# Optimization experiments

Hardware: AMD Instinct MI355X
Metric: run time of the kernel (lower is better)

Reference implementation:

```python
import jax, jax.numpy as jnp
import numpy as np

TOPK = 30  # from init_kwargs


def setup_inputs() -> dict:
    key = jax.random.key(0)
    k1, k2, k3 = jax.random.split(key, 3)
    BH, N, D = 32, 2048, 64  # (batch*heads, seq_len, head_dim)
    return {
        "q": jax.random.normal(k1, (BH, N, D), dtype=jnp.float32),
        "k": jax.random.normal(k2, (BH, N, D), dtype=jnp.float32),
        "v": jax.random.normal(k3, (BH, N, D), dtype=jnp.float32),
        "B": 2048,          # == seq_len N (used for mask shape in original)
        "num_heads": 8,     # unused by the math, kept for signature parity
    }


def reference(q, k, v, B, num_heads):
    # scores: [BH, N, N]  (torch.bmm(q, k.transpose(1,2)))
    scores = jnp.einsum('bnd,bmd->bnm', q, k)
    # scale=None and attn_mask=None in the default call -> both branches skipped
    BH, N, _ = scores.shape
    # top-k per row, scatter 1.0 into a zero mask (faithful to torch.scatter_)
    _, idx = jax.lax.top_k(scores, TOPK)                      # [BH, N, TOPK]
    bi = jnp.arange(BH)[:, None, None]
    ri = jnp.arange(N)[None, :, None]
    keep = jnp.zeros((BH, N, N), dtype=bool).at[bi, ri, idx].set(True)
    # masked softmax over last axis (dim=2)
    masked = jnp.where(keep, scores, -jnp.inf)
    attn = jax.nn.softmax(masked, axis=-1)
    # dropout p=0.0 -> identity
    context = jnp.einsum('bnm,bmd->bnd', attn, v)
    return context, attn
```

## Files before the change

kernel.cpp:

```cpp
#include <hip/hip_runtime.h>
#include <hip/hip_bf16.h>

#define BHn 32
#define Nn 2048
#define Dn 64
#define KSEL 30
#define CAP 92
#define RB 64
#define CT 64
#define ZTH 1.90f

typedef short bf16x8 __attribute__((ext_vector_type(8)));
typedef float f32x4 __attribute__((ext_vector_type(4)));
typedef unsigned long long u64;

__device__ __forceinline__ unsigned ford(float x) {
  unsigned b = __float_as_uint(x);
  return (b & 0x80000000u) ? ~b : (b | 0x80000000u);
}
__device__ __forceinline__ float unford(unsigned u) {
  unsigned b = (u & 0x80000000u) ? (u & 0x7fffffffu) : ~u;
  return __uint_as_float(b);
}
__device__ __forceinline__ u64 umax64(u64 a, u64 b) { return a > b ? a : b; }

__device__ __forceinline__ void split2(float a, float b, ushort2& hi, ushort2& lo) {
  __hip_bfloat162 h = __float22bfloat162_rn(make_float2(a, b));
  union { __hip_bfloat162 v; ushort2 u; } ch; ch.v = h;
  hi = ch.u;
  float2 hf = __bfloat1622float2(h);
  __hip_bfloat162 l = __float22bfloat162_rn(make_float2(a - hf.x, b - hf.y));
  union { __hip_bfloat162 v; ushort2 u; } cl; cl.v = l;
  lo = cl.u;
}

__device__ __forceinline__ void pack8(float4 x0, float4 x1, bf16x8& hi, bf16x8& lo) {
  ushort2 h0, l0, h1, l1, h2, l2, h3, l3;
  split2(x0.x, x0.y, h0, l0); split2(x0.z, x0.w, h1, l1);
  split2(x1.x, x1.y, h2, l2); split2(x1.z, x1.w, h3, l3);
  hi = (bf16x8){(short)h0.x, (short)h0.y, (short)h1.x, (short)h1.y,
                (short)h2.x, (short)h2.y, (short)h3.x, (short)h3.y};
  lo = (bf16x8){(short)l0.x, (short)l0.y, (short)l1.x, (short)l1.y,
                (short)l2.x, (short)l2.y, (short)l3.x, (short)l3.y};
}

__global__ __launch_bounds__(256, 2) void score_select(
    const float* __restrict__ q, const float* __restrict__ k,
    const float* __restrict__ v, float* __restrict__ ctx,
    float* __restrict__ attn, unsigned* __restrict__ flags) {
  __shared__ ushort kh[CT][64], kl[CT][64];
  __shared__ u64 candL[RB][CAP];
  __shared__ unsigned ccnt[RB];
  __shared__ float tf[RB];

  const int t = threadIdx.x;
  const int bid = blockIdx.x;
  const int bh = (bid & 7) * 4 + ((bid >> 3) & 3);
  const int rb = bid >> 5;
  const int lane = t & 63, w = t >> 6;
  const int m16 = lane & 15, quad = lane >> 4;
  const int wr = w >> 1, wc = w & 1;

  const float* qb = q + ((size_t)bh * Nn + rb * RB) * Dn;
  const float* kb = k + (size_t)bh * Nn * Dn;
  const size_t growbase = (size_t)bh * Nn + (size_t)rb * RB;

  bf16x8 qaH[2][2], qaL[2][2];
#pragma unroll
  for (int ks = 0; ks < 2; ++ks)
#pragma unroll
    for (int mt = 0; mt < 2; ++mt) {
      const float* p = qb + (wr * 32 + mt * 16 + m16) * Dn + (ks * 4 + quad) * 8;
      float4 x0 = *(const float4*)p;
      float4 x1 = *(const float4*)(p + 4);
      pack8(x0, x1, qaH[ks][mt], qaL[ks][mt]);
    }

  if (t < RB) {
    const float* qr = qb + t * Dn;
    float ss = 0.f;
#pragma unroll
    for (int i = 0; i < 16; ++i) {
      float4 a = *(const float4*)(qr + i * 4);
      ss = fmaf(a.x, a.x, ss); ss = fmaf(a.y, a.y, ss);
      ss = fmaf(a.z, a.z, ss); ss = fmaf(a.w, a.w, ss);
    }
    tf[t] = ZTH * sqrtf(ss);
    ccnt[t] = 0u;
  }

  float4 pre[4];
#pragma unroll
  for (int i = 0; i < 4; ++i) {
    int c = t + 256 * i;
    pre[i] = *(const float4*)(kb + (size_t)(c >> 4) * Dn + (c & 15) * 4);
  }
  __syncthreads();

  unsigned tfr[2][4];
#pragma unroll
  for (int mt = 0; mt < 2; ++mt)
#pragma unroll
    for (int rg = 0; rg < 4; ++rg)
      tfr[mt][rg] = ford(tf[wr * 32 + mt * 16 + quad * 4 + rg]);

  for (int ct = 0; ct < Nn / CT; ++ct) {
#pragma unroll
    for (int i = 0; i < 4; ++i) {
      int c = t + 256 * i;
      int row = c >> 4, f4 = c & 15;
      float4 a = pre[i];
      int sp = (((f4 >> 1) ^ (row & 7)) << 1) | (f4 & 1);
      ushort2 h0, l0, h1, l1;
      split2(a.x, a.y, h0, l0);
      split2(a.z, a.w, h1, l1);
      *(ushort4*)&kh[row][sp * 4] = make_ushort4(h0.x, h0.y, h1.x, h1.y);
      *(ushort4*)&kl[row][sp * 4] = make_ushort4(l0.x, l0.y, l1.x, l1.y);
    }
    __syncthreads();

    if (ct + 1 < Nn / CT) {
#pragma unroll
      for (int i = 0; i < 4; ++i) {
        int c = t + 256 * i;
        pre[i] = *(const float4*)(kb + (size_t)((ct + 1) * CT + (c >> 4)) * Dn + (c & 15) * 4);
      }
    }

    f32x4 acc[2][2];
#pragma unroll
    for (int mt = 0; mt < 2; ++mt)
#pragma unroll
      for (int nt = 0; nt < 2; ++nt) acc[mt][nt] = (f32x4){0.f, 0.f, 0.f, 0.f};

#pragma unroll
    for (int ks = 0; ks < 2; ++ks) {
      bf16x8 bH[2], bL[2];
#pragma unroll
      for (int nt = 0; nt < 2; ++nt) {
        int rr = wc * 32 + nt * 16 + m16;
        int ch = (ks * 4 + quad) ^ (rr & 7);
        bH[nt] = *(const bf16x8*)&kh[rr][ch * 8];
        bL[nt] = *(const bf16x8*)&kl[rr][ch * 8];
      }
#pragma unroll
      for (int mt = 0; mt < 2; ++mt)
#pragma unroll
        for (int nt = 0; nt < 2; ++nt) {
          acc[mt][nt] = __builtin_amdgcn_mfma_f32_16x16x32_bf16(qaL[ks][mt], bH[nt], acc[mt][nt], 0, 0, 0);
          acc[mt][nt] = __builtin_amdgcn_mfma_f32_16x16x32_bf16(qaH[ks][mt], bL[nt], acc[mt][nt], 0, 0, 0);
          acc[mt][nt] = __builtin_amdgcn_mfma_f32_16x16x32_bf16(qaH[ks][mt], bH[nt], acc[mt][nt], 0, 0, 0);
        }
    }

#pragma unroll
    for (int mt = 0; mt < 2; ++mt)
#pragma unroll
      for (int rg = 0; rg < 4; ++rg) {
        unsigned tk = tfr[mt][rg];
        int rl = wr * 32 + mt * 16 + quad * 4 + rg;
#pragma unroll
        for (int nt = 0; nt < 2; ++nt) {
          float s = acc[mt][nt][rg];
          unsigned fk = ford(s);
          if (fk > tk) {
            unsigned pos = atomicAdd(&ccnt[rl], 1u);
            if (pos < CAP) {
              int col = ct * CT + wc * 32 + nt * 16 + m16;
              candL[rl][pos] = ((u64)fk << 32) | (unsigned)(2047 - col);
            }
          }
        }
      }
    __syncthreads();
  }

  const float* vb = v + (size_t)bh * Nn * Dn;
  for (int i = 0; i < RB / 4; ++i) {
    const int rl = w * 16 + i;
    const size_t gr = growbase + rl;
    const int C = (int)ccnt[rl];
    const bool bad = (C < KSEL) || (C > CAP);
    if (lane == 0) flags[gr] = bad ? 1u : 0u;
    float* ab = attn + gr * (size_t)Nn;

    const f32x4 Z = (f32x4){0.f, 0.f, 0.f, 0.f};
#pragma unroll
    for (int jj = 0; jj < 8; ++jj)
      __builtin_nontemporal_store(Z, (f32x4*)(ab + jj * 256 + lane * 4));

    if (!bad) {
      u64* sw_ = &candL[rl][0];
      const int slots = (C + 63) >> 6;
      u64 mykey[2] = {0ull, 0ull};
      int rk[2] = {CAP, CAP};
      float es[2] = {0.f, 0.f};
      u64 mymax = 0ull;
#pragma unroll
      for (int tt = 0; tt < 2; ++tt) {
        if (tt < slots) {
          int p = lane + 64 * tt;
          mykey[tt] = (p < C) ? sw_[p] : 0ull;
          mymax = umax64(mymax, mykey[tt]);
        }
      }
#pragma unroll
      for (int off = 32; off; off >>= 1) mymax = umax64(mymax, __shfl_xor(mymax, off));
      const float mrow = unford((unsigned)(mymax >> 32));

#pragma unroll 1
      for (int tt = 0; tt < slots; ++tt) {
        int r = 0;
        u64 me = mykey[tt];
        for (int jj = 0; jj < C; ++jj) r += (sw_[jj] > me);
        rk[tt] = r;
      }
      float z = 0.f;
#pragma unroll
      for (int tt = 0; tt < 2; ++tt) {
        int p = lane + 64 * tt;
        bool sel = (tt < slots) && (p < C) && (rk[tt] < KSEL);
        es[tt] = sel ? __expf(unford((unsigned)(mykey[tt] >> 32)) - mrow) : 0.f;
        z += es[tt];
      }
#pragma unroll
      for (int off = 32; off; off >>= 1) z += __shfl_xor(z, off);
      const float invZ = 1.f / z;

#pragma unroll
      for (int tt = 0; tt < 2; ++tt) {
        int p = lane + 64 * tt;
        if (tt < slots && p < C && rk[tt] < KSEL) {
          float wt = es[tt] * invZ;
          int col = 2047 - (int)(mykey[tt] & 0xffffffffu);
          sw_[rk[tt]] = ((u64)__float_as_uint(wt) << 32) | (unsigned)col;
        }
      }
      float a = 0.f;
#pragma unroll
      for (int p = 0; p < KSEL; ++p) {
        u64 e = sw_[p];
        a = fmaf(__uint_as_float((unsigned)(e >> 32)), vb[(e & 0x7ffull) * Dn + lane], a);
      }
      ctx[gr * Dn + lane] = a;

      asm volatile("s_waitcnt vmcnt(0)" ::: "memory");
#pragma unroll
      for (int tt = 0; tt < 2; ++tt) {
        int p = lane + 64 * tt;
        if (tt < slots && p < C && rk[tt] < KSEL) {
          float wt = es[tt] * invZ;
          int col = 2047 - (int)(mykey[tt] & 0xffffffffu);
          __builtin_nontemporal_store(wt, ab + col);
        }
      }
    }
  }
}

__global__ __launch_bounds__(256) void repair_rows(
    const float* __restrict__ q, const float* __restrict__ k,
    const float* __restrict__ v, float* __restrict__ ctx,
    float* __restrict__ attn, const unsigned* __restrict__ flags) {
  __shared__ float sc2[Nn];
  __shared__ u64 red[256];
  __shared__ float qrow[Dn];
  __shared__ int selc[KSEL];
  __shared__ float selv[KSEL];
  __shared__ float zsh;
  __shared__ unsigned flagbuf[256];

  const int t = threadIdx.x;
  const int base = blockIdx.x * 256;
  flagbuf[t] = flags[base + t];
  __syncthreads();

  for (int i = 0; i < 256; ++i) {
    if (flagbuf[i] == 0u) continue;
    const int gr = base + i;
    const int bh = gr >> 11;
    if (t < Dn) qrow[t] = q[(size_t)gr * Dn + t];
    __syncthreads();
    const float* kb = k + (size_t)bh * Nn * Dn;
#pragma unroll
    for (int j = 0; j < 8; ++j) {
      int col = t + 256 * j;
      float s = 0.f;
      for (int d = 0; d < Dn; d += 4) {
        float4 kk = *(const float4*)(kb + (size_t)col * Dn + d);
        s = fmaf(qrow[d], kk.x, s);
        s = fmaf(qrow[d + 1], kk.y, s);
        s = fmaf(qrow[d + 2], kk.z, s);
        s = fmaf(qrow[d + 3], kk.w, s);
      }
      sc2[col] = s;
    }
    __syncthreads();
    for (int p = 0; p < KSEL; ++p) {
      u64 best = 0ull;
#pragma unroll
      for (int j = 0; j < 8; ++j) {
        int col = t + 256 * j;
        u64 kk = ((u64)ford(sc2[col]) << 32) | (unsigned)(2047 - col);
        best = umax64(best, kk);
      }
      red[t] = best;
      __syncthreads();
      for (int off = 128; off; off >>= 1) {
        if (t < off) red[t] = umax64(red[t], red[t + off]);
        __syncthreads();
      }
      if (t == 0) {
        u64 b = red[0];
        int col = 2047 - (int)(b & 0xffffffffu);
        selc[p] = col;
        selv[p] = unford((unsigned)(b >> 32));
        sc2[col] = -3.4e38f;
      }
      __syncthreads();
    }
    if (t == 0) {
      float m = selv[0], zz = 0.f;
      for (int p = 0; p < KSEL; ++p) zz += __expf(selv[p] - m);
      zsh = 1.f / zz;
    }
    __syncthreads();
    if (t < KSEL)
      attn[(size_t)gr * Nn + selc[t]] = __expf(selv[t] - selv[0]) * zsh;
    if (t < Dn) {
      const float* vb = v + (size_t)bh * Nn * Dn;
      float a = 0.f;
      for (int p = 0; p < KSEL; ++p)
        a = fmaf(__expf(selv[p] - selv[0]) * zsh, vb[(size_t)selc[p] * Dn + t], a);
      ctx[(size_t)gr * Dn + t] = a;
    }
    __syncthreads();
  }
}

extern "C" void kernel_launch(void* const* d_in, const int* in_sizes, int n_in,
                              void* d_out, int out_size, void* d_ws,
                              size_t ws_size, hipStream_t stream) {
  const float* q = (const float*)d_in[0];
  const float* k = (const float*)d_in[1];
  const float* v = (const float*)d_in[2];
  float* out = (float*)d_out;
  float* ctx = out;
  float* attn = out + (size_t)BHn * Nn * Dn;

  unsigned* flags = (unsigned*)d_ws;

  score_select<<<dim3(BHn * Nn / RB), 256, 0, stream>>>(q, k, v, ctx, attn, flags);
  repair_rows<<<dim3(BHn * Nn / 256), 256, 0, stream>>>(q, k, v, ctx, attn, flags);
}
```

Baseline: 881.3 us.

## Halve row block, remap waves across key columns, batch attn zeroing stores

Reduces the query row block from 64 to 32 and raises launch bounds to 4 blocks per CU. Each wave now covers all 32 rows against a 16-column slice of the key tile, so it needs fewer accumulators and less LDS for candidates. The epilogue now issues all zero-fill stores for the block's rows first, waits on memory once, and then scatters the selected attention weights, instead of waiting once per row. In exchange, each K tile is loaded and split into bf16 hi/lo twice as often overall, and the host grid must scale with RB.

```diff
diff --git a/kernel.cpp b/kernel.cpp
--- a/kernel.cpp
+++ b/kernel.cpp
@@ -6,7 +6,7 @@
 #define Dn 64
 #define KSEL 30
 #define CAP 92
-#define RB 64
+#define RB 32
 #define CT 64
 #define ZTH 1.90f
 
@@ -44,7 +44,7 @@
                 (short)l2.x, (short)l2.y, (short)l3.x, (short)l3.y};
 }
 
-__global__ __launch_bounds__(256, 2) void score_select(
+__global__ __launch_bounds__(256, 4) void score_select(
     const float* __restrict__ q, const float* __restrict__ k,
     const float* __restrict__ v, float* __restrict__ ctx,
     float* __restrict__ attn, unsigned* __restrict__ flags) {
@@ -59,7 +59,7 @@
   const int rb = bid >> 5;
   const int lane = t & 63, w = t >> 6;
   const int m16 = lane & 15, quad = lane >> 4;
-  const int wr = w >> 1, wc = w & 1;
+  const int wc = w;
 
   const float* qb = q + ((size_t)bh * Nn + rb * RB) * Dn;
   const float* kb = k + (size_t)bh * Nn * Dn;
@@ -70,7 +70,7 @@
   for (int ks = 0; ks < 2; ++ks)
 #pragma unroll
     for (int mt = 0; mt < 2; ++mt) {
-      const float* p = qb + (wr * 32 + mt * 16 + m16) * Dn + (ks * 4 + quad) * 8;
+      const float* p = qb + (mt * 16 + m16) * Dn + (ks * 4 + quad) * 8;
       float4 x0 = *(const float4*)p;
       float4 x1 = *(const float4*)(p + 4);
       pack8(x0, x1, qaH[ks][mt], qaL[ks][mt]);
@@ -102,7 +102,7 @@
   for (int mt = 0; mt < 2; ++mt)
 #pragma unroll
     for (int rg = 0; rg < 4; ++rg)
-      tfr[mt][rg] = ford(tf[wr * 32 + mt * 16 + quad * 4 + rg]);
+      tfr[mt][rg] = ford(tf[mt * 16 + quad * 4 + rg]);
 
   for (int ct = 0; ct < Nn / CT; ++ct) {
 #pragma unroll
@@ -127,30 +127,22 @@
       }
     }
 
-    f32x4 acc[2][2];
-#pragma unroll
-    for (int mt = 0; mt < 2; ++mt)
-#pragma unroll
-      for (int nt = 0; nt < 2; ++nt) acc[mt][nt] = (f32x4){0.f, 0.f, 0.f, 0.f};
+    f32x4 acc[2];
+#pragma unroll
+    for (int mt = 0; mt < 2; ++mt) acc[mt] = (f32x4){0.f, 0.f, 0.f, 0.f};
 
 #pragma unroll
     for (int ks = 0; ks < 2; ++ks) {
-      bf16x8 bH[2], bL[2];
-#pragma unroll
-      for (int nt = 0; nt < 2; ++nt) {
-        int rr = wc * 32 + nt * 16 + m16;
-        int ch = (ks * 4 + quad) ^ (rr & 7);
-        bH[nt] = *(const bf16x8*)&kh[rr][ch * 8];
-        bL[nt] = *(const bf16x8*)&kl[rr][ch * 8];
-      }
-#pragma unroll
-      for (int mt = 0; mt < 2; ++mt)
-#pragma unroll
-        for (int nt = 0; nt < 2; ++nt) {
-          acc[mt][nt] = __builtin_amdgcn_mfma_f32_16x16x32_bf16(qaL[ks][mt], bH[nt], acc[mt][nt], 0, 0, 0);
-          acc[mt][nt] = __builtin_amdgcn_mfma_f32_16x16x32_bf16(qaH[ks][mt], bL[nt], acc[mt][nt], 0, 0, 0);
-          acc[mt][nt] = __builtin_amdgcn_mfma_f32_16x16x32_bf16(qaH[ks][mt], bH[nt], acc[mt][nt], 0, 0, 0);
-        }
+      int rr = wc * 16 + m16;
+      int ch = (ks * 4 + quad) ^ (rr & 7);
+      bf16x8 bH = *(const bf16x8*)&kh[rr][ch * 8];
+      bf16x8 bL = *(const bf16x8*)&kl[rr][ch * 8];
+#pragma unroll
+      for (int mt = 0; mt < 2; ++mt) {
+        acc[mt] = __builtin_amdgcn_mfma_f32_16x16x32_bf16(qaL[ks][mt], bH, acc[mt], 0, 0, 0);
+        acc[mt] = __builtin_amdgcn_mfma_f32_16x16x32_bf16(qaH[ks][mt], bL, acc[mt], 0, 0, 0);
+        acc[mt] = __builtin_amdgcn_mfma_f32_16x16x32_bf16(qaH[ks][mt], bH, acc[mt], 0, 0, 0);
+      }
     }
 
 #pragma unroll
@@ -158,17 +150,14 @@
 #pragma unroll
       for (int rg = 0; rg < 4; ++rg) {
         unsigned tk = tfr[mt][rg];
-        int rl = wr * 32 + mt * 16 + quad * 4 + rg;
-#pragma unroll
-        for (int nt = 0; nt < 2; ++nt) {
-          float s = acc[mt][nt][rg];
-          unsigned fk = ford(s);
-          if (fk > tk) {
-            unsigned pos = atomicAdd(&ccnt[rl], 1u);
-            if (pos < CAP) {
-              int col = ct * CT + wc * 32 + nt * 16 + m16;
-              candL[rl][pos] = ((u64)fk << 32) | (unsigned)(2047 - col);
-            }
+        int rl = mt * 16 + quad * 4 + rg;
+        float s = acc[mt][rg];
+        unsigned fk = ford(s);
+        if (fk > tk) {
+          unsigned pos = atomicAdd(&ccnt[rl], 1u);
+          if (pos < CAP) {
+            int col = ct * CT + wc * 16 + m16;
+            candL[rl][pos] = ((u64)fk << 32) | (unsigned)(2047 - col);
           }
         }
       }
@@ -176,18 +165,23 @@
   }
 
   const float* vb = v + (size_t)bh * Nn * Dn;
+  const f32x4 Z = (f32x4){0.f, 0.f, 0.f, 0.f};
+
+#pragma unroll
   for (int i = 0; i < RB / 4; ++i) {
-    const int rl = w * 16 + i;
+    const size_t gr = growbase + w * (RB / 4) + i;
+    float* ab = attn + gr * (size_t)Nn;
+#pragma unroll
+    for (int jj = 0; jj < 8; ++jj)
+      __builtin_nontemporal_store(Z, (f32x4*)(ab + jj * 256 + lane * 4));
+  }
+
+  for (int i = 0; i < RB / 4; ++i) {
+    const int rl = w * (RB / 4) + i;
     const size_t gr = growbase + rl;
     const int C = (int)ccnt[rl];
     const bool bad = (C < KSEL) || (C > CAP);
     if (lane == 0) flags[gr] = bad ? 1u : 0u;
-    float* ab = attn + gr * (size_t)Nn;
-
-    const f32x4 Z = (f32x4){0.f, 0.f, 0.f, 0.f};
-#pragma unroll
-    for (int jj = 0; jj < 8; ++jj)
-      __builtin_nontemporal_store(Z, (f32x4*)(ab + jj * 256 + lane * 4));
 
     if (!bad) {
       u64* sw_ = &candL[rl][0];
@@ -243,17 +237,21 @@
         a = fmaf(__uint_as_float((unsigned)(e >> 32)), vb[(e & 0x7ffull) * Dn + lane], a);
       }
       ctx[gr * Dn + lane] = a;
-
-      asm volatile("s_waitcnt vmcnt(0)" ::: "memory");
-#pragma unroll
-      for (int tt = 0; tt < 2; ++tt) {
-        int p = lane + 64 * tt;
-        if (tt < slots && p < C && rk[tt] < KSEL) {
-          float wt = es[tt] * invZ;
-          int col = 2047 - (int)(mykey[tt] & 0xffffffffu);
-          __builtin_nontemporal_store(wt, ab + col);
-        }
-      }
+    }
+  }
+
+  asm volatile("s_waitcnt vmcnt(0)" ::: "memory");
+
+#pragma unroll 1
+  for (int i = 0; i < RB / 4; ++i) {
+    const int rl = w * (RB / 4) + i;
+    const size_t gr = growbase + rl;
+    const int C = (int)ccnt[rl];
+    if (C >= KSEL && C <= CAP && lane < KSEL) {
+      u64 e = candL[rl][lane];
+      float wt = __uint_as_float((unsigned)(e >> 32));
+      int col = (int)(e & 0x7ffull);
+      __builtin_nontemporal_store(wt, attn + gr * (size_t)Nn + col);
     }
   }
 }
```

Result: faster. 808.8 us (-8.2%).
